# Optimization experiments

Hardware: AMD Instinct MI355X
Metric: run time of the kernel (lower is better)

The kernel has to match this reference:

```python
import jax, jax.numpy as jnp
import numpy as np

NEG_BIG = 1e9


def setup_inputs() -> dict:
    key = jax.random.key(0)
    k1, k2, k3, k4 = jax.random.split(key, 4)
    B, N, M, D = 4, 512, 512, 128
    x = jax.random.normal(k1, (B, N, D), dtype=jnp.float32)
    y = jax.random.normal(k2, (B, M, D), dtype=jnp.float32)
    # lengths in [64, 512] so every example has a non-empty alignment region
    x_length = jax.random.randint(k3, (B,), 64, N + 1, dtype=jnp.int64)
    y_length = jax.random.randint(k4, (B,), 64, M + 1, dtype=jnp.int64)
    return {"x": x, "y": y, "x_length": x_length, "y_length": y_length}


def reference(x, y, x_length, y_length):
    B, N, D = x.shape
    M = y.shape[1]
    # sequence masks from lengths
    x_mask = jnp.arange(N)[None, :] < x_length[:, None]          # [B, N]
    y_mask = jnp.arange(M)[None, :] < y_length[:, None]          # [B, M]
    attention_mask = (x_mask[:, :, None] & y_mask[:, None, :]).astype(x.dtype)  # [B, N, M]
    # pairwise L1 distance: [B, N, M]
    z_diff = jnp.sum(jnp.abs(x[:, :, None, :] - y[:, None, :, :]), axis=-1)
    weights = -z_diff - NEG_BIG * (1.0 - attention_mask)
    alpha = jax.nn.softmax(weights, axis=1)  # over x positions
    beta = jax.nn.softmax(weights, axis=2)   # over y positions
    a = attention_mask * (alpha + beta - alpha * beta)
    ssa = -jnp.sum(a * z_diff, axis=(1, 2)) / jnp.sum(a, axis=(1, 2))  # [B]
    return ssa
```

## Files before the change

kernel.cpp:

```cpp
#include <hip/hip_runtime.h>


constexpr int B = 4, N = 512, M = 512, D = 128;
constexpr int TN = 64, TM = 64;
constexpr int LSTR = D + 4;
constexpr int NSLOT = 16;
#define SENT -3.0e38f

__device__ __forceinline__ int load_len(const int* p, int b) {
  bool is64 = (p[1] == 0) && (p[3] == 0);
  return is64 ? p[2 * b] : p[b];
}

__device__ __forceinline__ void compute_tile(const float* __restrict__ x,
                                             const float* __restrict__ y,
                                             int b, int n0, int m0, int tid,
                                             float* xs, float* ys,
                                             float zr[4][4]) {
  const float4* xg = (const float4*)(x + (size_t)(b * N + n0) * D);
  const float4* yg = (const float4*)(y + (size_t)(b * M + m0) * D);
#pragma unroll
  for (int k = 0; k < 8; ++k) {
    int idx = tid + k * 256;
    int r = idx >> 5;
    int c = (idx & 31) << 2;
    *(float4*)&xs[r * LSTR + c] = xg[idx];
    *(float4*)&ys[r * LSTR + c] = yg[idx];
  }
  __syncthreads();

  const int tx = tid & 15;
  const int ty = tid >> 4;
#pragma unroll
  for (int i = 0; i < 4; ++i)
#pragma unroll
    for (int j = 0; j < 4; ++j) zr[i][j] = 0.f;

#pragma unroll 4
  for (int dd = 0; dd < D; dd += 4) {
    float4 xa[4], yb[4];
#pragma unroll
    for (int i = 0; i < 4; ++i) xa[i] = *(const float4*)&xs[(ty + 16 * i) * LSTR + dd];
#pragma unroll
    for (int j = 0; j < 4; ++j) yb[j] = *(const float4*)&ys[(tx + 16 * j) * LSTR + dd];
#pragma unroll
    for (int i = 0; i < 4; ++i)
#pragma unroll
      for (int j = 0; j < 4; ++j) {
        zr[i][j] += fabsf(xa[i].x - yb[j].x);
        zr[i][j] += fabsf(xa[i].y - yb[j].y);
        zr[i][j] += fabsf(xa[i].z - yb[j].z);
        zr[i][j] += fabsf(xa[i].w - yb[j].w);
      }
  }
}

__global__ __launch_bounds__(256) void k1_stats(const float* __restrict__ x,
                                                const float* __restrict__ y,
                                                const int* __restrict__ xlen,
                                                const int* __restrict__ ylen,
                                                float2* __restrict__ rp,
                                                float2* __restrict__ cp,
                                                float* __restrict__ acc,
                                                float* __restrict__ zt_all) {
  __shared__ float xs[TN * LSTR];
  __shared__ float ys[TM * LSTR];
  __shared__ float2 colp[4][TM];
  const int b  = blockIdx.z;
  const int n0 = blockIdx.y * TN;
  const int m0 = blockIdx.x * TM;
  const int tid = threadIdx.x;
  const int xl = load_len(xlen, b);
  const int yl = load_len(ylen, b);

  if (blockIdx.x == 0 && blockIdx.y == 0 && blockIdx.z == 0 && tid < 2 * B * NSLOT)
    acc[tid] = 0.f;

  float zr[4][4];
  compute_tile(x, y, b, n0, m0, tid, xs, ys, zr);

  float* zt = zt_all + ((size_t)((b * 8 + (n0 >> 6)) * 8 + (m0 >> 6))) * (TN * TM);
#pragma unroll
  for (int i = 0; i < 4; ++i)
    *(float4*)&zt[(i * 256 + tid) * 4] =
        make_float4(zr[i][0], zr[i][1], zr[i][2], zr[i][3]);

  const int tx = tid & 15;
  const int ty = tid >> 4;
  const int wv = tid >> 6;

#pragma unroll
  for (int i = 0; i < 4; ++i) {
    float lm = SENT;
#pragma unroll
    for (int j = 0; j < 4; ++j)
      if (m0 + tx + 16 * j < yl) lm = fmaxf(lm, -zr[i][j]);
#pragma unroll
    for (int off = 1; off <= 8; off <<= 1) lm = fmaxf(lm, __shfl_xor(lm, off, 64));
    float ls = 0.f;
#pragma unroll
    for (int j = 0; j < 4; ++j)
      if (m0 + tx + 16 * j < yl) ls += __expf(-zr[i][j] - lm);
#pragma unroll
    for (int off = 1; off <= 8; off <<= 1) ls += __shfl_xor(ls, off, 64);
    if (tx == 0)
      rp[((b * 8 + (m0 >> 6)) * N) + n0 + ty + 16 * i] = make_float2(lm, ls);
  }

#pragma unroll
  for (int j = 0; j < 4; ++j) {
    float cm = SENT;
#pragma unroll
    for (int i = 0; i < 4; ++i)
      if (n0 + ty + 16 * i < xl) cm = fmaxf(cm, -zr[i][j]);
    cm = fmaxf(cm, __shfl_xor(cm, 16, 64));
    cm = fmaxf(cm, __shfl_xor(cm, 32, 64));
    float cs = 0.f;
#pragma unroll
    for (int i = 0; i < 4; ++i)
      if (n0 + ty + 16 * i < xl) cs += __expf(-zr[i][j] - cm);
    cs += __shfl_xor(cs, 16, 64);
    cs += __shfl_xor(cs, 32, 64);
    if ((ty & 3) == 0) colp[wv][tx + 16 * j] = make_float2(cm, cs);
  }
  __syncthreads();
  if (tid < TM) {
    float2 p0 = colp[0][tid], p1 = colp[1][tid], p2 = colp[2][tid], p3 = colp[3][tid];
    float gm = fmaxf(fmaxf(p0.x, p1.x), fmaxf(p2.x, p3.x));
    float gs = p0.y * __expf(p0.x - gm) + p1.y * __expf(p1.x - gm) +
               p2.y * __expf(p2.x - gm) + p3.y * __expf(p3.x - gm);
    cp[((b * 8 + (n0 >> 6)) * M) + m0 + tid] = make_float2(gm, gs);
  }
}

__global__ __launch_bounds__(256) void k2_final(const int* __restrict__ xlen,
                                                const int* __restrict__ ylen,
                                                const float2* __restrict__ rp,
                                                const float2* __restrict__ cp,
                                                const float* __restrict__ zt_all,
                                                float* __restrict__ acc) {
  __shared__ float rm_s[TN], ri_s[TN], cm_s[TM], ci_s[TM];
  __shared__ float red[4][2];
  const int b  = blockIdx.z;
  const int n0 = blockIdx.y * TN;
  const int m0 = blockIdx.x * TM;
  const int tid = threadIdx.x;
  const int xl = load_len(xlen, b);
  const int yl = load_len(ylen, b);

  const float* zt = zt_all + ((size_t)((b * 8 + (n0 >> 6)) * 8 + (m0 >> 6))) * (TN * TM);
  float4 zv[4];
#pragma unroll
  for (int i = 0; i < 4; ++i) zv[i] = *(const float4*)&zt[(i * 256 + tid) * 4];

  if (tid < 128) {
    bool isrow = tid < 64;
    int p = isrow ? (n0 + tid) : (m0 + tid - 64);
    const float2* src = isrow ? rp : cp;
    float2 v[8];
    float gm = SENT;
#pragma unroll
    for (int t = 0; t < 8; ++t) {
      v[t] = src[(b * 8 + t) * 512 + p];
      gm = fmaxf(gm, v[t].x);
    }
    float gs = 0.f;
#pragma unroll
    for (int t = 0; t < 8; ++t) gs += v[t].y * __expf(v[t].x - gm);
    float inv = 1.0f / gs;
    if (isrow) { rm_s[tid] = gm; ri_s[tid] = inv; }
    else       { cm_s[tid - 64] = gm; ci_s[tid - 64] = inv; }
  }
  __syncthreads();

  const int tx = tid & 15;
  const int ty = tid >> 4;
  float num = 0.f, den = 0.f;
#pragma unroll
  for (int i = 0; i < 4; ++i) {
    int nl = ty + 16 * i;
    if (n0 + nl >= xl) continue;
    float rm = rm_s[nl], ri = ri_s[nl];
    float zrow[4] = {zv[i].x, zv[i].y, zv[i].z, zv[i].w};
#pragma unroll
    for (int j = 0; j < 4; ++j) {
      int ml = tx + 16 * j;
      if (m0 + ml >= yl) continue;
      float zval = zrow[j];
      float w = -zval;
      float alpha = __expf(w - cm_s[ml]) * ci_s[ml];
      float beta  = __expf(w - rm) * ri;
      float a = alpha + beta - alpha * beta;
      num += a * zval;
      den += a;
    }
  }
#pragma unroll
  for (int off = 32; off > 0; off >>= 1) {
    num += __shfl_xor(num, off, 64);
    den += __shfl_xor(den, off, 64);
  }
  if ((tid & 63) == 0) { red[tid >> 6][0] = num; red[tid >> 6][1] = den; }
  __syncthreads();
  if (tid == 0) {
    int slot = (blockIdx.x + blockIdx.y) & (NSLOT - 1);
    atomicAdd(&acc[b * NSLOT + slot],
              red[0][0] + red[1][0] + red[2][0] + red[3][0]);
    atomicAdd(&acc[(B + b) * NSLOT + slot],
              red[0][1] + red[1][1] + red[2][1] + red[3][1]);
  }
}

__global__ void k3_out(const float* __restrict__ acc, float* __restrict__ out) {
  int l = threadIdx.x;
  float a = acc[l];
  float d = acc[64 + l];
#pragma unroll
  for (int off = 1; off <= 8; off <<= 1) {
    a += __shfl_xor(a, off, 64);
    d += __shfl_xor(d, off, 64);
  }
  if ((l & 15) == 0) out[l >> 4] = -a / d;
}

extern "C" void kernel_launch(void* const* d_in, const int* in_sizes, int n_in,
                              void* d_out, int out_size, void* d_ws, size_t ws_size,
                              hipStream_t stream) {
  const float* x    = (const float*)d_in[0];
  const float* y    = (const float*)d_in[1];
  const int*   xlen = (const int*)d_in[2];
  const int*   ylen = (const int*)d_in[3];
  float* out = (float*)d_out;

  float* ws = (float*)d_ws;
  float2* rp  = (float2*)ws;              size_t off = (size_t)B * 8 * N * 2;
  float2* cp  = (float2*)(ws + off);      off += (size_t)B * 8 * M * 2;
  float*  acc = ws + off;                 off += 2 * B * NSLOT;
  float*  zt  = ws + off;                 off += (size_t)B * 8 * 8 * TN * TM;

  k1_stats<<<dim3(M / TM, N / TN, B), 256, 0, stream>>>(x, y, xlen, ylen, rp, cp, acc, zt);
  k2_final<<<dim3(M / TM, N / TN, B), 256, 0, stream>>>(xlen, ylen, rp, cp, zt, acc);
  k3_out<<<1, 64, 0, stream>>>(acc, out);
}
```

Before: 82.72 us.

## Use 32x32 tiles and skip fully masked tiles in both passes

Halves the tile size to 32x32, so the grid grows to 16x16 tiles per batch, and returns early from any block whose tile lies entirely beyond the x or y length. The second pass merges row and column softmax partials online, reading only the tiles that hold valid data. This cuts out distance and softmax work on padded regions and spreads the work over more blocks. In exchange each thread computes only a 2x2 register tile, which lowers reuse of each shared-memory load, and there are more partial statistics to merge.

New measurement: 82.24 us. About the same (-0.6%).

```diff
diff --git a/kernel.cpp b/kernel.cpp
--- a/kernel.cpp
+++ b/kernel.cpp
@@ -2,7 +2,8 @@
 
 
 constexpr int B = 4, N = 512, M = 512, D = 128;
-constexpr int TN = 64, TM = 64;
+constexpr int TN = 32, TM = 32;
+constexpr int NT = 16;
 constexpr int LSTR = D + 4;
 constexpr int NSLOT = 16;
 #define SENT -3.0e38f
@@ -10,49 +11,6 @@
 __device__ __forceinline__ int load_len(const int* p, int b) {
   bool is64 = (p[1] == 0) && (p[3] == 0);
   return is64 ? p[2 * b] : p[b];
-}
-
-__device__ __forceinline__ void compute_tile(const float* __restrict__ x,
-                                             const float* __restrict__ y,
-                                             int b, int n0, int m0, int tid,
-                                             float* xs, float* ys,
-                                             float zr[4][4]) {
-  const float4* xg = (const float4*)(x + (size_t)(b * N + n0) * D);
-  const float4* yg = (const float4*)(y + (size_t)(b * M + m0) * D);
-#pragma unroll
-  for (int k = 0; k < 8; ++k) {
-    int idx = tid + k * 256;
-    int r = idx >> 5;
-    int c = (idx & 31) << 2;
-    *(float4*)&xs[r * LSTR + c] = xg[idx];
-    *(float4*)&ys[r * LSTR + c] = yg[idx];
-  }
-  __syncthreads();
-
-  const int tx = tid & 15;
-  const int ty = tid >> 4;
-#pragma unroll
-  for (int i = 0; i < 4; ++i)
-#pragma unroll
-    for (int j = 0; j < 4; ++j) zr[i][j] = 0.f;
-
-#pragma unroll 4
-  for (int dd = 0; dd < D; dd += 4) {
-    float4 xa[4], yb[4];
-#pragma unroll
-    for (int i = 0; i < 4; ++i) xa[i] = *(const float4*)&xs[(ty + 16 * i) * LSTR + dd];
-#pragma unroll
-    for (int j = 0; j < 4; ++j) yb[j] = *(const float4*)&ys[(tx + 16 * j) * LSTR + dd];
-#pragma unroll
-    for (int i = 0; i < 4; ++i)
-#pragma unroll
-      for (int j = 0; j < 4; ++j) {
-        zr[i][j] += fabsf(xa[i].x - yb[j].x);
-        zr[i][j] += fabsf(xa[i].y - yb[j].y);
-        zr[i][j] += fabsf(xa[i].z - yb[j].z);
-        zr[i][j] += fabsf(xa[i].w - yb[j].w);
-      }
-  }
 }
 
 __global__ __launch_bounds__(256) void k1_stats(const float* __restrict__ x,
@@ -76,48 +34,80 @@
   if (blockIdx.x == 0 && blockIdx.y == 0 && blockIdx.z == 0 && tid < 2 * B * NSLOT)
     acc[tid] = 0.f;
 
-  float zr[4][4];
-  compute_tile(x, y, b, n0, m0, tid, xs, ys, zr);
-
-  float* zt = zt_all + ((size_t)((b * 8 + (n0 >> 6)) * 8 + (m0 >> 6))) * (TN * TM);
-#pragma unroll
-  for (int i = 0; i < 4; ++i)
-    *(float4*)&zt[(i * 256 + tid) * 4] =
-        make_float4(zr[i][0], zr[i][1], zr[i][2], zr[i][3]);
+  if (n0 >= xl || m0 >= yl) return;
+
+  {
+    const float4* xg = (const float4*)(x + (size_t)(b * N + n0) * D);
+    const float4* yg = (const float4*)(y + (size_t)(b * M + m0) * D);
+#pragma unroll
+    for (int k = 0; k < 4; ++k) {
+      int idx = tid + k * 256;
+      int r = idx >> 5;
+      int c = (idx & 31) << 2;
+      *(float4*)&xs[r * LSTR + c] = xg[idx];
+      *(float4*)&ys[r * LSTR + c] = yg[idx];
+    }
+  }
+  __syncthreads();
 
   const int tx = tid & 15;
   const int ty = tid >> 4;
+  float zr[2][2] = {{0.f, 0.f}, {0.f, 0.f}};
+
+#pragma unroll 4
+  for (int dd = 0; dd < D; dd += 4) {
+    float4 xa[2], yb[2];
+#pragma unroll
+    for (int i = 0; i < 2; ++i) xa[i] = *(const float4*)&xs[(ty + 16 * i) * LSTR + dd];
+#pragma unroll
+    for (int j = 0; j < 2; ++j) yb[j] = *(const float4*)&ys[(tx + 16 * j) * LSTR + dd];
+#pragma unroll
+    for (int i = 0; i < 2; ++i)
+#pragma unroll
+      for (int j = 0; j < 2; ++j) {
+        zr[i][j] += fabsf(xa[i].x - yb[j].x);
+        zr[i][j] += fabsf(xa[i].y - yb[j].y);
+        zr[i][j] += fabsf(xa[i].z - yb[j].z);
+        zr[i][j] += fabsf(xa[i].w - yb[j].w);
+      }
+  }
+
+  float* zt = zt_all + ((size_t)((b * NT + (n0 >> 5)) * NT + (m0 >> 5))) * (TN * TM);
+#pragma unroll
+  for (int i = 0; i < 2; ++i)
+    *(float2*)&zt[(i * 256 + tid) * 2] = make_float2(zr[i][0], zr[i][1]);
+
   const int wv = tid >> 6;
 
 #pragma unroll
-  for (int i = 0; i < 4; ++i) {
+  for (int i = 0; i < 2; ++i) {
     float lm = SENT;
 #pragma unroll
-    for (int j = 0; j < 4; ++j)
+    for (int j = 0; j < 2; ++j)
       if (m0 + tx + 16 * j < yl) lm = fmaxf(lm, -zr[i][j]);
 #pragma unroll
     for (int off = 1; off <= 8; off <<= 1) lm = fmaxf(lm, __shfl_xor(lm, off, 64));
     float ls = 0.f;
 #pragma unroll
-    for (int j = 0; j < 4; ++j)
+    for (int j = 0; j < 2; ++j)
       if (m0 + tx + 16 * j < yl) ls += __expf(-zr[i][j] - lm);
 #pragma unroll
     for (int off = 1; off <= 8; off <<= 1) ls += __shfl_xor(ls, off, 64);
     if (tx == 0)
-      rp[((b * 8 + (m0 >> 6)) * N) + n0 + ty + 16 * i] = make_float2(lm, ls);
-  }
-
-#pragma unroll
-  for (int j = 0; j < 4; ++j) {
+      rp[((b * NT + (m0 >> 5)) * N) + n0 + ty + 16 * i] = make_float2(lm, ls);
+  }
+
+#pragma unroll
+  for (int j = 0; j < 2; ++j) {
     float cm = SENT;
 #pragma unroll
-    for (int i = 0; i < 4; ++i)
+    for (int i = 0; i < 2; ++i)
       if (n0 + ty + 16 * i < xl) cm = fmaxf(cm, -zr[i][j]);
     cm = fmaxf(cm, __shfl_xor(cm, 16, 64));
     cm = fmaxf(cm, __shfl_xor(cm, 32, 64));
     float cs = 0.f;
 #pragma unroll
-    for (int i = 0; i < 4; ++i)
+    for (int i = 0; i < 2; ++i)
       if (n0 + ty + 16 * i < xl) cs += __expf(-zr[i][j] - cm);
     cs += __shfl_xor(cs, 16, 64);
     cs += __shfl_xor(cs, 32, 64);
@@ -129,7 +119,7 @@
     float gm = fmaxf(fmaxf(p0.x, p1.x), fmaxf(p2.x, p3.x));
     float gs = p0.y * __expf(p0.x - gm) + p1.y * __expf(p1.x - gm) +
                p2.y * __expf(p2.x - gm) + p3.y * __expf(p3.x - gm);
-    cp[((b * 8 + (n0 >> 6)) * M) + m0 + tid] = make_float2(gm, gs);
+    cp[((b * NT + (n0 >> 5)) * M) + m0 + tid] = make_float2(gm, gs);
   }
 }
 
@@ -148,28 +138,31 @@
   const int xl = load_len(xlen, b);
   const int yl = load_len(ylen, b);
 
-  const float* zt = zt_all + ((size_t)((b * 8 + (n0 >> 6)) * 8 + (m0 >> 6))) * (TN * TM);
-  float4 zv[4];
-#pragma unroll
-  for (int i = 0; i < 4; ++i) zv[i] = *(const float4*)&zt[(i * 256 + tid) * 4];
-
-  if (tid < 128) {
-    bool isrow = tid < 64;
-    int p = isrow ? (n0 + tid) : (m0 + tid - 64);
+  if (n0 >= xl || m0 >= yl) return;
+
+  const int ntm = (yl + 31) >> 5;
+  const int ntn = (xl + 31) >> 5;
+
+  const float* zt = zt_all + ((size_t)((b * NT + (n0 >> 5)) * NT + (m0 >> 5))) * (TN * TM);
+  float2 zv[2];
+#pragma unroll
+  for (int i = 0; i < 2; ++i) zv[i] = *(const float2*)&zt[(i * 256 + tid) * 2];
+
+  if (tid < 64) {
+    bool isrow = tid < 32;
+    int p = isrow ? (n0 + tid) : (m0 + tid - 32);
+    int cnt = isrow ? ntm : ntn;
     const float2* src = isrow ? rp : cp;
-    float2 v[8];
-    float gm = SENT;
-#pragma unroll
-    for (int t = 0; t < 8; ++t) {
-      v[t] = src[(b * 8 + t) * 512 + p];
-      gm = fmaxf(gm, v[t].x);
+    float gm = SENT, gs = 0.f;
+    for (int t = 0; t < cnt; ++t) {
+      float2 v = src[(b * NT + t) * 512 + p];
+      float nm = fmaxf(gm, v.x);
+      gs = gs * __expf(gm - nm) + v.y * __expf(v.x - nm);
+      gm = nm;
     }
-    float gs = 0.f;
-#pragma unroll
-    for (int t = 0; t < 8; ++t) gs += v[t].y * __expf(v[t].x - gm);
     float inv = 1.0f / gs;
     if (isrow) { rm_s[tid] = gm; ri_s[tid] = inv; }
-    else       { cm_s[tid - 64] = gm; ci_s[tid - 64] = inv; }
+    else       { cm_s[tid - 32] = gm; ci_s[tid - 32] = inv; }
   }
   __syncthreads();
 
@@ -177,13 +170,13 @@
   const int ty = tid >> 4;
   float num = 0.f, den = 0.f;
 #pragma unroll
-  for (int i = 0; i < 4; ++i) {
+  for (int i = 0; i < 2; ++i) {
     int nl = ty + 16 * i;
     if (n0 + nl >= xl) continue;
     float rm = rm_s[nl], ri = ri_s[nl];
-    float zrow[4] = {zv[i].x, zv[i].y, zv[i].z, zv[i].w};
-#pragma unroll
-    for (int j = 0; j < 4; ++j) {
+    float zrow[2] = {zv[i].x, zv[i].y};
+#pragma unroll
+    for (int j = 0; j < 2; ++j) {
       int ml = tx + 16 * j;
       if (m0 + ml >= yl) continue;
       float zval = zrow[j];
@@ -233,10 +226,10 @@
   float* out = (float*)d_out;
 
   float* ws = (float*)d_ws;
-  float2* rp  = (float2*)ws;              size_t off = (size_t)B * 8 * N * 2;
-  float2* cp  = (float2*)(ws + off);      off += (size_t)B * 8 * M * 2;
+  float2* rp  = (float2*)ws;              size_t off = (size_t)B * NT * N * 2;
+  float2* cp  = (float2*)(ws + off);      off += (size_t)B * NT * M * 2;
   float*  acc = ws + off;                 off += 2 * B * NSLOT;
-  float*  zt  = ws + off;                 off += (size_t)B * 8 * 8 * TN * TM;
+  float*  zt  = ws + off;                 off += (size_t)B * NT * NT * TN * TM;
 
   k1_stats<<<dim3(M / TM, N / TN, B), 256, 0, stream>>>(x, y, xlen, ylen, rp, cp, acc, zt);
   k2_final<<<dim3(M / TM, N / TN, B), 256, 0, stream>>>(xlen, ylen, rp, cp, zt, acc);
```
